# Optimization experiments

Measured on AMD Instinct MI355X. Metric: run time of the kernel, lower is better.

The kernel has to match this reference:

```python
import jax, jax.numpy as jnp
import numpy as np

D = 1024
H = 16
HD = D // H
FFN = D * 2
EPS = 1e-5


def _layernorm(x, g, b):
    mu = jnp.mean(x, axis=-1, keepdims=True)
    var = jnp.var(x, axis=-1, keepdims=True)
    return (x - mu) * jax.lax.rsqrt(var + EPS) * g + b


def setup_inputs() -> dict:
    key = jax.random.key(0)
    ks = jax.random.split(key, 12)
    s = 1.0 / np.sqrt(D)
    inp = {
        "x": jax.random.normal(ks[0], (2, 2048, D), dtype=jnp.float32),
        "Wq": jax.random.normal(ks[1], (D, D), dtype=jnp.float32) * s,
        "bq": jnp.zeros((D,), jnp.float32),
        "Wk": jax.random.normal(ks[2], (D, D), dtype=jnp.float32) * s,
        "bk": jnp.zeros((D,), jnp.float32),
        "Wv": jax.random.normal(ks[3], (D, D), dtype=jnp.float32) * s,
        "bv": jnp.zeros((D,), jnp.float32),
        "Wo": jax.random.normal(ks[4], (D, D), dtype=jnp.float32) * s,
        "bo": jnp.zeros((D,), jnp.float32),
        "g1": jnp.ones((D,), jnp.float32),
        "b1": jnp.zeros((D,), jnp.float32),
        "W_ff1": jax.random.normal(ks[5], (D, FFN), dtype=jnp.float32) * s,
        "b_ff1": jnp.zeros((FFN,), jnp.float32),
        "W_ff2": jax.random.normal(ks[6], (FFN, D), dtype=jnp.float32) * (1.0 / np.sqrt(FFN)),
        "b_ff2": jnp.zeros((D,), jnp.float32),
        "g2": jnp.ones((D,), jnp.float32),
        "b2": jnp.zeros((D,), jnp.float32),
    }
    return inp


def reference(x, Wq, bq, Wk, bk, Wv, bv, Wo, bo, g1, b1, W_ff1, b_ff1, W_ff2, b_ff2, g2, b2):
    B, S, _ = x.shape
    # QKV projections -> [B, H, S, HD]
    def split_heads(t):
        return t.reshape(B, S, H, HD).transpose(0, 2, 1, 3)
    Q = split_heads(x @ Wq + bq)
    K = split_heads(x @ Wk + bk)
    V = split_heads(x @ Wv + bv)
    scores = jnp.einsum('bhqd,bhkd->bhqk', Q, K) / np.sqrt(HD).astype(np.float32)
    attn = jax.nn.softmax(scores, axis=-1)  # dropout = identity in eval
    ctx = jnp.einsum('bhqk,bhkd->bhqd', attn, V)
    ctx = ctx.transpose(0, 2, 1, 3).reshape(B, S, D)
    x = _layernorm(x + ctx @ Wo + bo, g1, b1)
    h = jax.nn.gelu(x @ W_ff1 + b_ff1, approximate=False)
    x = _layernorm(x + h @ W_ff2 + b_ff2, g2, b2)
    return x
```

## Files before the change

kernel.cpp:

```cpp
#include <hip/hip_runtime.h>

#define SEQ 2048
#define NTOK 4096
#define DM 1024
#define LDQK 3072

typedef __attribute__((ext_vector_type(4))) float f32x4;
typedef __attribute__((ext_vector_type(8))) short short8;
typedef __attribute__((ext_vector_type(4))) short short4v;

__device__ __forceinline__ short f2bf(float f) {
  union { float f; unsigned u; } x; x.f = f;
  unsigned r = x.u + 0x7fffu + ((x.u >> 16) & 1u);
  return (short)(r >> 16);
}

__device__ __forceinline__ void async_load16(const void* g, void* l) {
  __builtin_amdgcn_global_load_lds(
      (const __attribute__((address_space(1))) void*)g,
      (__attribute__((address_space(3))) void*)l, 16, 0, 0);
}

__global__ void __launch_bounds__(256) prep_all(
    const float* __restrict__ Wq, const float* __restrict__ Wk,
    const float* __restrict__ Wv, const float* __restrict__ Wo,
    const float* __restrict__ Wf1, const float* __restrict__ Wf2,
    const float* __restrict__ x,
    short* __restrict__ Wqkv, short* __restrict__ Wto,
    short* __restrict__ Wtf1, short* __restrict__ Wtf2,
    short* __restrict__ xb) {
  const int z = blockIdx.z;
  const int tx = threadIdx.x, ty = threadIdx.y;
  if (z == 6) {
    int blk = blockIdx.y * 64 + blockIdx.x;
    int i = blk * 256 + ty * 32 + tx;
    f32x4 v = ((const f32x4*)x)[i];
    short4v o;
#pragma unroll
    for (int j = 0; j < 4; ++j) o[j] = f2bf(v[j]);
    ((short4v*)xb)[i] = o;
    return;
  }
  const float* in;
  short* out;
  int K, N;
  switch (z) {
    case 0: in = Wq;  out = Wqkv;               K = 1024; N = 1024; break;
    case 1: in = Wk;  out = Wqkv + 1024 * 1024; K = 1024; N = 1024; break;
    case 2: in = Wv;  out = Wqkv + 2048 * 1024; K = 1024; N = 1024; break;
    case 3: in = Wo;  out = Wto;                K = 1024; N = 1024; break;
    case 4: in = Wf1; out = Wtf1;               K = 1024; N = 2048; break;
    default: in = Wf2; out = Wtf2;              K = 2048; N = 1024; break;
  }
  if (blockIdx.x * 32 >= N || blockIdx.y * 32 >= K) return;
  __shared__ float t[32][33];
  const int n = blockIdx.x * 32 + tx;
#pragma unroll
  for (int i = 0; i < 4; ++i) {
    int k = blockIdx.y * 32 + ty + i * 8;
    t[ty + i * 8][tx] = in[(size_t)k * N + n];
  }
  __syncthreads();
  const int k2 = blockIdx.y * 32 + tx;
#pragma unroll
  for (int i = 0; i < 4; ++i) {
    int n2 = blockIdx.x * 32 + ty + i * 8;
    out[(size_t)n2 * K + k2] = f2bf(t[tx][ty + i * 8]);
  }
}

template <int EPI, bool TRIPLE>
__global__ void __launch_bounds__(256, 2) gemm_bt(
    const short* __restrict__ A, const short* __restrict__ Bt,
    const float* __restrict__ b0, const float* __restrict__ b1,
    const float* __restrict__ b2, void* __restrict__ Cout,
    short* __restrict__ VtOut, int M, int N, int K) {
  __shared__ __align__(16) short As[128 * 64];
  __shared__ __align__(16) short Bs[128 * 64];
  const int w = threadIdx.x >> 6, lane = threadIdx.x & 63;
  const int hi = lane >> 4, lo = lane & 15;
  const int bm = blockIdx.y, bn = blockIdx.x;
  const int wr = w >> 1, wc = w & 1;
  f32x4 acc[4][4] = {};
  const int nkt = K >> 6;
  for (int kt = 0; kt < nkt; ++kt) {
#pragma unroll
    for (int j = 0; j < 4; ++j) {
      int c = (j * 4 + w) * 64 + lane;
      int r = c >> 3;
      int scc = (c & 7) ^ (r & 7);
      async_load16(A + (size_t)(bm * 128 + r) * K + kt * 64 + scc * 8,
                   &As[(j * 4 + w) * 512]);
      async_load16(Bt + (size_t)(bn * 128 + r) * K + kt * 64 + scc * 8,
                   &Bs[(j * 4 + w) * 512]);
    }
    __syncthreads();
#pragma unroll
    for (int ks = 0; ks < 2; ++ks) {
      short8 af[4], bf[4];
#pragma unroll
      for (int m = 0; m < 4; ++m) {
        int row = wr * 64 + m * 16 + lo;
        int ch = (ks * 4 + hi) ^ (row & 7);
        af[m] = *(const short8*)(&As[row * 64 + ch * 8]);
      }
#pragma unroll
      for (int n = 0; n < 4; ++n) {
        int row = wc * 64 + n * 16 + lo;
        int ch = (ks * 4 + hi) ^ (row & 7);
        bf[n] = *(const short8*)(&Bs[row * 64 + ch * 8]);
      }
#pragma unroll
      for (int m = 0; m < 4; ++m)
#pragma unroll
        for (int n = 0; n < 4; ++n)
          acc[m][n] = __builtin_amdgcn_mfma_f32_16x16x32_bf16(af[m], bf[n], acc[m][n], 0, 0, 0);
    }
    __syncthreads();
  }
  const float* bp = b0;
  if (TRIPLE) { int r = bn >> 3; bp = (r == 0) ? b0 : ((r == 1) ? b1 : b2); }
  const int colb = bn * 128 + wc * 64 + lo;
  if (TRIPLE && bn >= 16) {
#pragma unroll
    for (int m = 0; m < 4; ++m) {
      int row0 = bm * 128 + wr * 64 + m * 16 + hi * 4;
      int bb = row0 >> 11, ss = row0 & 2047;
#pragma unroll
      for (int n = 0; n < 4; ++n) {
        int col = colb + n * 16;
        int vdim = col - 2048;
        int hh = vdim >> 6, dd = vdim & 63;
        float bs = bp[vdim];
        short4v t;
#pragma unroll
        for (int j = 0; j < 4; ++j) t[j] = f2bf(acc[m][n][j] + bs);
        *(short4v*)&VtOut[((size_t)(bb * 16 + hh) * 64 + dd) * SEQ + ss] = t;
      }
    }
    return;
  }
#pragma unroll
  for (int m = 0; m < 4; ++m) {
    int row0 = bm * 128 + wr * 64 + m * 16 + hi * 4;
#pragma unroll
    for (int n = 0; n < 4; ++n) {
      int col = colb + n * 16;
      float bs = bp[TRIPLE ? (col & 1023) : col];
#pragma unroll
      for (int j = 0; j < 4; ++j) {
        float v = acc[m][n][j] + bs;
        if (EPI == 1) v = 0.5f * v * (1.f + erff(v * 0.70710678f));
        size_t idx = (size_t)(row0 + j) * N + col;
        if (EPI == 2) ((float*)Cout)[idx] = v;
        else ((short*)Cout)[idx] = f2bf(v);
      }
    }
  }
}

__global__ void __launch_bounds__(256, 2) gemm_n64(
    const short* __restrict__ A, const short* __restrict__ Bt,
    const float* __restrict__ b0, float* __restrict__ Cout,
    int M, int N, int K) {
  __shared__ __align__(16) short As[128 * 64];
  __shared__ __align__(16) short Bs[64 * 64];
  const int w = threadIdx.x >> 6, lane = threadIdx.x & 63;
  const int hi = lane >> 4, lo = lane & 15;
  const int bm = blockIdx.y, bn = blockIdx.x;
  const int wr = w >> 1, wc = w & 1;
  f32x4 acc[4][2] = {};
  const int nkt = K >> 6;
  for (int kt = 0; kt < nkt; ++kt) {
#pragma unroll
    for (int j = 0; j < 4; ++j) {
      int c = (j * 4 + w) * 64 + lane;
      int r = c >> 3;
      int scc = (c & 7) ^ (r & 7);
      async_load16(A + (size_t)(bm * 128 + r) * K + kt * 64 + scc * 8,
                   &As[(j * 4 + w) * 512]);
    }
#pragma unroll
    for (int j = 0; j < 2; ++j) {
      int c = j * 256 + w * 64 + lane;
      int r = c >> 3;
      int scc = (c & 7) ^ (r & 7);
      async_load16(Bt + (size_t)(bn * 64 + r) * K + kt * 64 + scc * 8,
                   &Bs[(j * 256 + w * 64) * 8]);
    }
    __syncthreads();
#pragma unroll
    for (int ks = 0; ks < 2; ++ks) {
      short8 af[4], bf[2];
#pragma unroll
      for (int m = 0; m < 4; ++m) {
        int row = wr * 64 + m * 16 + lo;
        int ch = (ks * 4 + hi) ^ (row & 7);
        af[m] = *(const short8*)(&As[row * 64 + ch * 8]);
      }
#pragma unroll
      for (int n = 0; n < 2; ++n) {
        int row = wc * 32 + n * 16 + lo;
        int ch = (ks * 4 + hi) ^ (row & 7);
        bf[n] = *(const short8*)(&Bs[row * 64 + ch * 8]);
      }
#pragma unroll
      for (int m = 0; m < 4; ++m)
#pragma unroll
        for (int n = 0; n < 2; ++n)
          acc[m][n] = __builtin_amdgcn_mfma_f32_16x16x32_bf16(af[m], bf[n], acc[m][n], 0, 0, 0);
    }
    __syncthreads();
  }
  const int colb = bn * 64 + wc * 32 + lo;
#pragma unroll
  for (int m = 0; m < 4; ++m) {
    int row0 = bm * 128 + wr * 64 + m * 16 + hi * 4;
#pragma unroll
    for (int n = 0; n < 2; ++n) {
      int col = colb + n * 16;
      float bs = b0[col];
#pragma unroll
      for (int j = 0; j < 4; ++j)
        Cout[(size_t)(row0 + j) * N + col] = acc[m][n][j] + bs;
    }
  }
}

__global__ void __launch_bounds__(256, 2) attn_kernel(
    const short* __restrict__ Qb, const short* __restrict__ Kb,
    const short* __restrict__ Vt, short* __restrict__ ctx) {
  const int w = threadIdx.x >> 6, lane = threadIdx.x & 63;
  const int hi = lane >> 4, lo = lane & 15;
  const int tid = threadIdx.x;
  const int L = blockIdx.y * 16 + blockIdx.x;
  const int W = (L & 7) * 64 + (L >> 3);
  const int qt = W & 15, bh = W >> 4;
  const int b = bh >> 4, h = bh & 15;
  const int qbase = qt * 128 + w * 32;
  const float C = 0.18033688f;

  __shared__ __align__(16) short Ks[128 * 64];
  __shared__ __align__(16) short Vs[64 * 128];
  __shared__ __align__(16) short P[4][16 * 128];

  const short* qp = Qb + (size_t)(b * SEQ + qbase + lo) * LDQK + h * 64;
  short8 bq[2][2];
#pragma unroll
  for (int u = 0; u < 2; ++u)
#pragma unroll
    for (int c = 0; c < 2; ++c)
      bq[u][c] = *(const short8*)(qp + (size_t)u * 16 * LDQK + c * 32 + hi * 8);

  const short* kb = Kb + (size_t)(b * SEQ) * LDQK + h * 64;
  const short* vb = Vt + (size_t)bh * 64 * SEQ;

  auto stage = [&](int kt) {
    const short* kg = kb + (size_t)(kt * 128) * LDQK;
#pragma unroll
    for (int i = 0; i < 4; ++i) {
      int c = i * 256 + tid;
      int r = c >> 3, scc = (c & 7) ^ (r & 7);
      async_load16(kg + (size_t)r * LDQK + scc * 8,
                   &Ks[(i * 256 + w * 64) * 8]);
    }
    const short* vg = vb + kt * 128;
#pragma unroll
    for (int i = 0; i < 4; ++i) {
      int c = i * 256 + tid;
      int r = c >> 4, sc2 = (c & 15) ^ (r & 7);
      async_load16(vg + (size_t)r * SEQ + sc2 * 8,
                   &Vs[(i * 256 + w * 64) * 8]);
    }
  };

  f32x4 o[2][4] = {};
  float lacc[2] = {0.f, 0.f};
  const int x7 = lo & 7;

  for (int kt = 0; kt < SEQ / 128; ++kt) {
    stage(kt);
    __syncthreads();

    f32x4 s[2][8] = {};
#pragma unroll
    for (int g = 0; g < 8; ++g) {
      const short* kr = &Ks[(g * 16 + lo) * 64];
      short8 ka0 = *(const short8*)(kr + ((hi) ^ x7) * 8);
      short8 ka1 = *(const short8*)(kr + ((4 + hi) ^ x7) * 8);
      s[0][g] = __builtin_amdgcn_mfma_f32_16x16x32_bf16(ka0, bq[0][0], s[0][g], 0, 0, 0);
      s[1][g] = __builtin_amdgcn_mfma_f32_16x16x32_bf16(ka0, bq[1][0], s[1][g], 0, 0, 0);
      s[0][g] = __builtin_amdgcn_mfma_f32_16x16x32_bf16(ka1, bq[0][1], s[0][g], 0, 0, 0);
      s[1][g] = __builtin_amdgcn_mfma_f32_16x16x32_bf16(ka1, bq[1][1], s[1][g], 0, 0, 0);
    }
    short8 vv[4][4];
#pragma unroll
    for (int ks = 0; ks < 4; ++ks)
#pragma unroll
      for (int a = 0; a < 4; ++a)
        vv[ks][a] = *(const short8*)(&Vs[(a * 16 + lo) * 128 + (((ks * 4 + hi) ^ x7) * 8)]);
#pragma unroll
    for (int u = 0; u < 2; ++u) {
      float rsg[8];
      short* pbase = &P[w][0];
#pragma unroll
      for (int g = 0; g < 8; ++g) {
        float p0 = exp2f(s[u][g][0] * C);
        float p1 = exp2f(s[u][g][1] * C);
        float p2 = exp2f(s[u][g][2] * C);
        float p3 = exp2f(s[u][g][3] * C);
        rsg[g] = (p0 + p1) + (p2 + p3);
        unsigned w0, w1;
        asm("v_cvt_pk_bf16_f32 %0, %1, %2" : "=v"(w0) : "v"(p0), "v"(p1));
        asm("v_cvt_pk_bf16_f32 %0, %1, %2" : "=v"(w1) : "v"(p2), "v"(p3));
        union { unsigned uu[2]; short4v s4; } cv;
        cv.uu[0] = w0; cv.uu[1] = w1;
        int pc = (2 * g + (hi >> 1)) ^ x7;
        *(short4v*)(pbase + lo * 128 + pc * 8 + (hi & 1) * 4) = cv.s4;
      }
#pragma unroll
      for (int ks = 0; ks < 4; ++ks) {
        int pc = (ks * 4 + hi) ^ x7;
        short8 pa = *(const short8*)(pbase + lo * 128 + pc * 8);
#pragma unroll
        for (int a = 0; a < 4; ++a)
          o[u][a] = __builtin_amdgcn_mfma_f32_16x16x32_bf16(pa, vv[ks][a], o[u][a], 0, 0, 0);
      }
      lacc[u] += ((rsg[0] + rsg[1]) + (rsg[2] + rsg[3])) +
                 ((rsg[4] + rsg[5]) + (rsg[6] + rsg[7]));
    }
    __syncthreads();
  }
#pragma unroll
  for (int u = 0; u < 2; ++u) {
    lacc[u] += __shfl_xor(lacc[u], 16);
    lacc[u] += __shfl_xor(lacc[u], 32);
  }
#pragma unroll
  for (int u = 0; u < 2; ++u)
#pragma unroll
    for (int j = 0; j < 4; ++j) {
      float lj = __shfl(lacc[u], hi * 4 + j);
      float inv = 1.f / lj;
      int row = qbase + u * 16 + hi * 4 + j;
#pragma unroll
      for (int a = 0; a < 4; ++a)
        ctx[(size_t)(b * SEQ + row) * DM + h * 64 + a * 16 + lo] = f2bf(o[u][a][j] * inv);
    }
}

__global__ void __launch_bounds__(256) residual_ln(
    const float* __restrict__ xr, const float* __restrict__ yr,
    const float* __restrict__ g, const float* __restrict__ beta,
    float* __restrict__ outf, short* __restrict__ outb) {
  const int row = blockIdx.x;
  const int t = threadIdx.x;
  const size_t base = (size_t)row * DM;
  f32x4 xv = ((const f32x4*)(xr + base))[t];
  f32x4 yv = ((const f32x4*)(yr + base))[t];
  f32x4 v = xv + yv;
  float s = v[0] + v[1] + v[2] + v[3];
  float s2 = v[0] * v[0] + v[1] * v[1] + v[2] * v[2] + v[3] * v[3];
#pragma unroll
  for (int off = 1; off < 64; off <<= 1) {
    s += __shfl_xor(s, off);
    s2 += __shfl_xor(s2, off);
  }
  __shared__ float rs[4], rs2[4];
  if ((t & 63) == 0) { rs[t >> 6] = s; rs2[t >> 6] = s2; }
  __syncthreads();
  s = rs[0] + rs[1] + rs[2] + rs[3];
  s2 = rs2[0] + rs2[1] + rs2[2] + rs2[3];
  float mu = s * (1.f / DM);
  float var = s2 * (1.f / DM) - mu * mu;
  float rstd = rsqrtf(var + 1e-5f);
  f32x4 gv = ((const f32x4*)g)[t];
  f32x4 bv = ((const f32x4*)beta)[t];
  f32x4 ov;
#pragma unroll
  for (int j = 0; j < 4; ++j) ov[j] = (v[j] - mu) * rstd * gv[j] + bv[j];
  ((f32x4*)(outf + base))[t] = ov;
  if (outb) {
    short4v sb;
#pragma unroll
    for (int j = 0; j < 4; ++j) sb[j] = f2bf(ov[j]);
    ((short4v*)(outb + base))[t] = sb;
  }
}

extern "C" void kernel_launch(void* const* d_in, const int* in_sizes, int n_in,
                              void* d_out, int out_size, void* d_ws, size_t ws_size,
                              hipStream_t stream) {
  (void)in_sizes; (void)n_in; (void)out_size; (void)ws_size;
  const float* x   = (const float*)d_in[0];
  const float* Wq  = (const float*)d_in[1];
  const float* bq  = (const float*)d_in[2];
  const float* Wk  = (const float*)d_in[3];
  const float* bk  = (const float*)d_in[4];
  const float* Wv  = (const float*)d_in[5];
  const float* bv  = (const float*)d_in[6];
  const float* Wo  = (const float*)d_in[7];
  const float* bo  = (const float*)d_in[8];
  const float* g1  = (const float*)d_in[9];
  const float* b1  = (const float*)d_in[10];
  const float* Wf1 = (const float*)d_in[11];
  const float* bf1 = (const float*)d_in[12];
  const float* Wf2 = (const float*)d_in[13];
  const float* bf2 = (const float*)d_in[14];
  const float* g2  = (const float*)d_in[15];
  const float* b2  = (const float*)d_in[16];

  char* ws = (char*)d_ws;
  const size_t MB = 1u << 20;
  short* Wqkv = (short*)(ws + 0 * MB);
  short* Wto  = (short*)(ws + 6 * MB);
  short* Wtf1 = (short*)(ws + 8 * MB);
  short* Wtf2 = (short*)(ws + 12 * MB);
  short* xb   = (short*)(ws + 16 * MB);
  short* QKV  = (short*)(ws + 24 * MB);
  short* Vt   = (short*)(ws + 48 * MB);
  short* ctxb = (short*)(ws + 56 * MB);
  float* aout = (float*)(ws + 64 * MB);
  float* x1f  = (float*)(ws + 80 * MB);
  short* x1b  = xb;
  short* hb   = QKV;
  float* ffo  = (float*)(ws + 48 * MB);

  prep_all<<<dim3(64, 64, 7), dim3(32, 8), 0, stream>>>(
      Wq, Wk, Wv, Wo, Wf1, Wf2, x, Wqkv, Wto, Wtf1, Wtf2, xb);

  gemm_bt<0, true><<<dim3(24, 32), 256, 0, stream>>>(
      xb, Wqkv, bq, bk, bv, QKV, Vt, NTOK, 3072, 1024);

  attn_kernel<<<dim3(16, 32), 256, 0, stream>>>(QKV, QKV + 1024, Vt, ctxb);

  gemm_n64<<<dim3(16, 32), 256, 0, stream>>>(ctxb, Wto, bo, aout, NTOK, 1024, 1024);
  residual_ln<<<4096, 256, 0, stream>>>(x, aout, g1, b1, x1f, x1b);
  gemm_bt<1, false><<<dim3(16, 32), 256, 0, stream>>>(
      x1b, Wtf1, bf1, bf1, bf1, hb, nullptr, NTOK, 2048, 1024);
  gemm_n64<<<dim3(16, 32), 256, 0, stream>>>(hb, Wtf2, bf2, ffo, NTOK, 1024, 2048);
  residual_ln<<<4096, 256, 0, stream>>>(x1f, ffo, g2, b2, (float*)d_out, nullptr);
}
```

Before: 229.9 us.

## Double-buffer K/V tiles in attention and store GEMM outputs as bf16

The attention kernel now keeps two LDS buffers for K and V. It issues the async loads for the next key tile before computing on the current one, so global-to-LDS transfers overlap the MFMA and softmax work instead of stalling at each iteration. The two gemm_n64 projections (attention output and FFN2) now write bf16 instead of fp32, and residual_ln reads bf16 and converts it back, roughly halving the traffic for those intermediates. The cost is more LDS per attention block, which may limit occupancy, and extra rounding before the residual add and layernorm.

```diff
diff --git a/kernel.cpp b/kernel.cpp
--- a/kernel.cpp
+++ b/kernel.cpp
@@ -13,6 +13,12 @@
   union { float f; unsigned u; } x; x.f = f;
   unsigned r = x.u + 0x7fffu + ((x.u >> 16) & 1u);
   return (short)(r >> 16);
+}
+
+__device__ __forceinline__ float bf2f(short s) {
+  union { unsigned u; float f; } x;
+  x.u = ((unsigned)(unsigned short)s) << 16;
+  return x.f;
 }
 
 __device__ __forceinline__ void async_load16(const void* g, void* l) {
@@ -151,9 +157,7 @@
       for (int j = 0; j < 4; ++j) {
         float v = acc[m][n][j] + bs;
         if (EPI == 1) v = 0.5f * v * (1.f + erff(v * 0.70710678f));
-        size_t idx = (size_t)(row0 + j) * N + col;
-        if (EPI == 2) ((float*)Cout)[idx] = v;
-        else ((short*)Cout)[idx] = f2bf(v);
+        ((short*)Cout)[(size_t)(row0 + j) * N + col] = f2bf(v);
       }
     }
   }
@@ -161,7 +165,7 @@
 
 __global__ void __launch_bounds__(256, 2) gemm_n64(
     const short* __restrict__ A, const short* __restrict__ Bt,
-    const float* __restrict__ b0, float* __restrict__ Cout,
+    const float* __restrict__ b0, short* __restrict__ Cout,
     int M, int N, int K) {
   __shared__ __align__(16) short As[128 * 64];
   __shared__ __align__(16) short Bs[64 * 64];
@@ -222,7 +226,7 @@
       float bs = b0[col];
 #pragma unroll
       for (int j = 0; j < 4; ++j)
-        Cout[(size_t)(row0 + j) * N + col] = acc[m][n][j] + bs;
+        Cout[(size_t)(row0 + j) * N + col] = f2bf(acc[m][n][j] + bs);
     }
   }
 }
@@ -240,8 +244,8 @@
   const int qbase = qt * 128 + w * 32;
   const float C = 0.18033688f;
 
-  __shared__ __align__(16) short Ks[128 * 64];
-  __shared__ __align__(16) short Vs[64 * 128];
+  __shared__ __align__(16) short Ks[2][128 * 64];
+  __shared__ __align__(16) short Vs[2][64 * 128];
   __shared__ __align__(16) short P[4][16 * 128];
 
   const short* qp = Qb + (size_t)(b * SEQ + qbase + lo) * LDQK + h * 64;
@@ -255,14 +259,14 @@
   const short* kb = Kb + (size_t)(b * SEQ) * LDQK + h * 64;
   const short* vb = Vt + (size_t)bh * 64 * SEQ;
 
-  auto stage = [&](int kt) {
+  auto stage = [&](int kt, int buf) {
     const short* kg = kb + (size_t)(kt * 128) * LDQK;
 #pragma unroll
     for (int i = 0; i < 4; ++i) {
       int c = i * 256 + tid;
       int r = c >> 3, scc = (c & 7) ^ (r & 7);
       async_load16(kg + (size_t)r * LDQK + scc * 8,
-                   &Ks[(i * 256 + w * 64) * 8]);
+                   &Ks[buf][(i * 256 + w * 64) * 8]);
     }
     const short* vg = vb + kt * 128;
 #pragma unroll
@@ -270,22 +274,25 @@
       int c = i * 256 + tid;
       int r = c >> 4, sc2 = (c & 15) ^ (r & 7);
       async_load16(vg + (size_t)r * SEQ + sc2 * 8,
-                   &Vs[(i * 256 + w * 64) * 8]);
+                   &Vs[buf][(i * 256 + w * 64) * 8]);
     }
   };
+
+  stage(0, 0);
+  __syncthreads();
 
   f32x4 o[2][4] = {};
   float lacc[2] = {0.f, 0.f};
   const int x7 = lo & 7;
 
   for (int kt = 0; kt < SEQ / 128; ++kt) {
-    stage(kt);
-    __syncthreads();
+    const int buf = kt & 1;
+    if (kt + 1 < SEQ / 128) stage(kt + 1, buf ^ 1);
 
     f32x4 s[2][8] = {};
 #pragma unroll
     for (int g = 0; g < 8; ++g) {
-      const short* kr = &Ks[(g * 16 + lo) * 64];
+      const short* kr = &Ks[buf][(g * 16 + lo) * 64];
       short8 ka0 = *(const short8*)(kr + ((hi) ^ x7) * 8);
       short8 ka1 = *(const short8*)(kr + ((4 + hi) ^ x7) * 8);
       s[0][g] = __builtin_amdgcn_mfma_f32_16x16x32_bf16(ka0, bq[0][0], s[0][g], 0, 0, 0);
@@ -298,7 +305,7 @@
     for (int ks = 0; ks < 4; ++ks)
 #pragma unroll
       for (int a = 0; a < 4; ++a)
-        vv[ks][a] = *(const short8*)(&Vs[(a * 16 + lo) * 128 + (((ks * 4 + hi) ^ x7) * 8)]);
+        vv[ks][a] = *(const short8*)(&Vs[buf][(a * 16 + lo) * 128 + (((ks * 4 + hi) ^ x7) * 8)]);
 #pragma unroll
     for (int u = 0; u < 2; ++u) {
       float rsg[8];
@@ -350,15 +357,17 @@
 }
 
 __global__ void __launch_bounds__(256) residual_ln(
-    const float* __restrict__ xr, const float* __restrict__ yr,
+    const float* __restrict__ xr, const short* __restrict__ yr,
     const float* __restrict__ g, const float* __restrict__ beta,
     float* __restrict__ outf, short* __restrict__ outb) {
   const int row = blockIdx.x;
   const int t = threadIdx.x;
   const size_t base = (size_t)row * DM;
   f32x4 xv = ((const f32x4*)(xr + base))[t];
-  f32x4 yv = ((const f32x4*)(yr + base))[t];
-  f32x4 v = xv + yv;
+  short4v yv4 = ((const short4v*)(yr + base))[t];
+  f32x4 v;
+#pragma unroll
+  for (int j = 0; j < 4; ++j) v[j] = xv[j] + bf2f(yv4[j]);
   float s = v[0] + v[1] + v[2] + v[3];
   float s2 = v[0] * v[0] + v[1] * v[1] + v[2] * v[2] + v[3] * v[3];
 #pragma unroll
@@ -420,11 +429,11 @@
   short* QKV  = (short*)(ws + 24 * MB);
   short* Vt   = (short*)(ws + 48 * MB);
   short* ctxb = (short*)(ws + 56 * MB);
-  float* aout = (float*)(ws + 64 * MB);
+  short* aout = (short*)(ws + 64 * MB);
   float* x1f  = (float*)(ws + 80 * MB);
   short* x1b  = xb;
   short* hb   = QKV;
-  float* ffo  = (float*)(ws + 48 * MB);
+  short* ffo  = (short*)(ws + 48 * MB);
 
   prep_all<<<dim3(64, 64, 7), dim3(32, 8), 0, stream>>>(
       Wq, Wk, Wv, Wo, Wf1, Wf2, x, Wqkv, Wto, Wtf1, Wtf2, xb);
```

After: 222.2 us. 3.4% less time.
